# Kernel optimization log

Measured on AMD Instinct MI355X. Metric: run time of the kernel, lower is better.

Reference implementation:

```python
import jax, jax.numpy as jnp
import numpy as np


def gcn_conv(x, W, b, src, dst, n_nodes):
    """PyG GCNConv: linear transform, then symmetric-normalized sparse aggregation.
    src/dst already include self-loops. Messages flow src -> dst."""
    xw = x @ W  # [N, out]
    deg = jax.ops.segment_sum(jnp.ones_like(dst, dtype=xw.dtype), dst, num_segments=n_nodes)
    dinv = jnp.where(deg > 0, jax.lax.rsqrt(deg), 0.0)
    norm = dinv[src] * dinv[dst]  # [E]
    msg = xw[src] * norm[:, None]  # gather + scale
    out = jax.ops.segment_sum(msg, dst, num_segments=n_nodes)  # scatter-add
    return out + b


def setup_inputs() -> dict:
    key = jax.random.key(0)
    ks = jax.random.split(key, 5)
    N, E, C_in, C_out = 50000, 800000, 512, 128
    H = 2 * C_out
    x = jax.random.normal(ks[0], (N, C_in), dtype=jnp.float32)
    edge_index = jax.random.randint(ks[1], (2, E), 0, N, dtype=jnp.int64)
    def glorot(k, shape):
        lim = float(np.sqrt(6.0 / (shape[0] + shape[1])))
        return jax.random.uniform(k, shape, jnp.float32, -lim, lim)
    return {
        "x": x,
        "edge_index": edge_index,
        "W1": glorot(ks[2], (C_in, H)),
        "b1": jnp.zeros((H,), jnp.float32),
        "W_mu": glorot(ks[3], (H, C_out)),
        "b_mu": jnp.zeros((C_out,), jnp.float32),
        "W_ls": glorot(ks[4], (H, C_out)),
        "b_ls": jnp.zeros((C_out,), jnp.float32),
    }


def reference(x, edge_index, W1, b1, W_mu, b_mu, W_ls, b_ls):
    n_nodes = x.shape[0]
    # add self-loops (PyG GCNConv default add_self_loops=True)
    loops = jnp.arange(n_nodes, dtype=edge_index.dtype)
    src = jnp.concatenate([edge_index[0], loops])
    dst = jnp.concatenate([edge_index[1], loops])
    h = jax.nn.relu(gcn_conv(x, W1, b1, src, dst, n_nodes))
    mu = gcn_conv(h, W_mu, b_mu, src, dst, n_nodes)
    logstd = gcn_conv(h, W_ls, b_ls, src, dst, n_nodes)
    # stack so output is a single array [2, N, out_channels]
    return jnp.stack([mu, logstd])
```

## Files before the change

kernel.cpp:

```cpp
#include <hip/hip_runtime.h>

static inline int ceil_div(int a, int b) { return (a + b - 1) / b; }

typedef __attribute__((ext_vector_type(8))) __bf16 bf16x8;
typedef __attribute__((ext_vector_type(8))) unsigned short ushort8;
typedef __attribute__((ext_vector_type(4))) float f32x4;

#define ELLPAD 64

__device__ __forceinline__ unsigned short f2bf(float f) {
    union { float f; unsigned u; } v; v.f = f;
    unsigned r = v.u + 0x7fffu + ((v.u >> 16) & 1u);
    return (unsigned short)(r >> 16);
}
__device__ __forceinline__ float blo(unsigned u) {
    union { unsigned u; float f; } x; x.u = u << 16; return x.f;
}
__device__ __forceinline__ float bhi(unsigned u) {
    union { unsigned u; float f; } x; x.u = u & 0xffff0000u; return x.f;
}

#define SWZ(r) ((((r) & 3) ^ (((r) >> 2) & 3)))

typedef __attribute__((address_space(3))) unsigned lds_uint;
typedef __attribute__((address_space(1))) const unsigned glb_uint;
__device__ __forceinline__ void gload_lds16(const unsigned short* g, unsigned short* l) {
    __builtin_amdgcn_global_load_lds((glb_uint*)g, (lds_uint*)l, 16, 0, 0);
}

__global__ __launch_bounds__(256) void k_prep(const int* __restrict__ src, const int* __restrict__ dst,
                                              int E, int* __restrict__ cnt, int* __restrict__ ell, int N,
                                              const float* __restrict__ x, unsigned short* __restrict__ xb,
                                              long nx,
                                              const float* __restrict__ W1, const float* __restrict__ Wmu,
                                              const float* __restrict__ Wls, unsigned short* __restrict__ W1t,
                                              unsigned short* __restrict__ Wct, int K1, int H, int Cout,
                                              int nbE, int nbX, int ilv) {
    const int b = blockIdx.x;
    int phase, idx;
    if (b < nbE + nbX) {
        if (ilv) {
            if ((b % 5) == 0 && (b / 5) < nbE) { phase = 0; idx = b / 5; }
            else { phase = 1; idx = b - min(b / 5 + 1, nbE); }
        } else {
            if (b < nbE) { phase = 0; idx = b; }
            else { phase = 1; idx = b - nbE; }
        }
    } else { phase = 2; idx = b - nbE - nbX; }

    if (phase == 0) {
        const int e = idx * 256 + threadIdx.x;
        if (e < E) {
            const int d = dst[e];
            const int r = atomicAdd(&cnt[d], 1);
            if (r < ELLPAD) ell[(size_t)d * ELLPAD + r] = src[e];
        }
    } else if (phase == 1) {
        long i = (long)idx * 2048 + (long)threadIdx.x * 8;
        if (i < nx) {
            float4 a0 = *(const float4*)(x + i);
            float4 a1 = *(const float4*)(x + i + 4);
            ushort8 t;
            t[0] = f2bf(a0.x); t[1] = f2bf(a0.y); t[2] = f2bf(a0.z); t[3] = f2bf(a0.w);
            t[4] = f2bf(a1.x); t[5] = f2bf(a1.y); t[6] = f2bf(a1.z); t[7] = f2bf(a1.w);
            *(ushort8*)(xb + i) = t;
        }
    } else {
        int t = idx * 256 + threadIdx.x;
        int n1 = H * K1;
        int n2 = 2 * Cout * H;
        if (t < n1) {
            int c = t / K1, k = t - c * K1;
            W1t[t] = f2bf(W1[(size_t)k * H + c]);
        } else if (t < n1 + n2) {
            int u = t - n1;
            int c = u / H, k = u - c * H;
            float v = (c < Cout) ? Wmu[(size_t)k * Cout + c] : Wls[(size_t)k * Cout + (c - Cout)];
            Wct[u] = f2bf(v);
        }
    }
}

__device__ __forceinline__ void gemm_tile_core(const unsigned short* __restrict__ A,
                                               const unsigned short* __restrict__ B,
                                               unsigned short* __restrict__ As, unsigned short* __restrict__ Bs,
                                               int row0, int col0, int K,
                                               int wave, int lane, f32x4 (*acc)[4]) {
    const int quad = lane >> 4, l16 = lane & 15;
    const int rw = wave & 1, cw = wave >> 1;
    const int srow = wave * 32 + (lane >> 2);
    const int slot = lane & 3;
    for (int k0 = 0; k0 < K; k0 += 32) {
#pragma unroll
        for (int t = 0; t < 2; ++t) {
            const int lr = srow + t * 16;
            const int kc = (slot ^ SWZ(lr)) * 8;
            gload_lds16(A + (size_t)(row0 + lr) * K + k0 + kc, As + (wave * 32 + t * 16) * 32);
            gload_lds16(B + (size_t)(col0 + lr) * K + k0 + kc, Bs + (wave * 32 + t * 16) * 32);
        }
        __syncthreads();
        bf16x8 af[4], bf[4];
#pragma unroll
        for (int i = 0; i < 4; ++i) {
            const int lr = rw * 64 + i * 16 + l16;
            af[i] = *(const bf16x8*)&As[lr * 32 + ((quad ^ SWZ(lr))) * 8];
            const int lc = cw * 64 + i * 16 + l16;
            bf[i] = *(const bf16x8*)&Bs[lc * 32 + ((quad ^ SWZ(lc))) * 8];
        }
#pragma unroll
        for (int i = 0; i < 4; ++i)
#pragma unroll
            for (int j = 0; j < 4; ++j)
                acc[i][j] = __builtin_amdgcn_mfma_f32_16x16x32_bf16(af[i], bf[j], acc[i][j], 0, 0, 0);
        __syncthreads();
    }
}

__global__ __launch_bounds__(256) void k_gemm1(const unsigned short* __restrict__ xb,
                                               const unsigned short* __restrict__ W1t,
                                               unsigned short* __restrict__ y, int N, int K,
                                               const int* __restrict__ cnt, float* __restrict__ dinv) {
    __shared__ __align__(16) unsigned short As[128 * 32];
    __shared__ __align__(16) unsigned short Bs[128 * 32];
    const int tid = threadIdx.x, wave = tid >> 6, lane = tid & 63;
    const int quad = lane >> 4, l16 = lane & 15;
    const int row0 = blockIdx.x * 128, col0 = blockIdx.y * 128;
    if (blockIdx.y == 0 && tid < 128) {
        const int i = row0 + tid;
        if (i < N) dinv[i] = rsqrtf((float)(cnt[i] + 1));
    }
    const int rw = wave & 1, cw = wave >> 1;
    f32x4 acc[4][4] = {};
    gemm_tile_core(xb, W1t, As, Bs, row0, col0, K, wave, lane, acc);
#pragma unroll
    for (int i = 0; i < 4; ++i) {
        const int grb = row0 + rw * 64 + i * 16 + quad * 4;
#pragma unroll
        for (int r = 0; r < 4; ++r) {
            const int row = grb + r;
            if (row < N) {
#pragma unroll
                for (int j = 0; j < 4; ++j)
                    y[(size_t)row * 256 + col0 + cw * 64 + j * 16 + l16] = f2bf(acc[i][j][r]);
            }
        }
    }
}

__global__ __launch_bounds__(256) void k_gemm2(const unsigned short* __restrict__ g,
                                               const unsigned short* __restrict__ Wct,
                                               const float* __restrict__ bmu, const float* __restrict__ bls,
                                               float* __restrict__ out, int N, int Cout) {
    __shared__ __align__(16) unsigned short As[128 * 32];
    __shared__ __align__(16) unsigned short Bs[128 * 32];
    const int K = 256;
    const int tid = threadIdx.x, wave = tid >> 6, lane = tid & 63;
    const int quad = lane >> 4, l16 = lane & 15;
    const int row0 = blockIdx.x * 128, col0 = blockIdx.y * 128;
    const int rw = wave & 1, cw = wave >> 1;
    f32x4 acc[4][4] = {};
    gemm_tile_core(g, Wct, As, Bs, row0, col0, K, wave, lane, acc);
#pragma unroll
    for (int j = 0; j < 4; ++j) {
        const int c = col0 + cw * 64 + j * 16 + l16;
        const bool is_mu = (c < Cout);
        const int ocl = is_mu ? c : (c - Cout);
        const float bv = is_mu ? bmu[ocl] : bls[ocl];
        const size_t obase = is_mu ? 0 : (size_t)N * Cout;
#pragma unroll
        for (int i = 0; i < 4; ++i) {
            const int grb = row0 + rw * 64 + i * 16 + quad * 4;
#pragma unroll
            for (int r = 0; r < 4; ++r) {
                const int row = grb + r;
                if (row < N) out[obase + (size_t)row * Cout + ocl] = acc[i][j][r] + bv;
            }
        }
    }
}

__global__ __launch_bounds__(256) void k_agg(const unsigned short* __restrict__ Yin,
                                             const int* __restrict__ ell, const int* __restrict__ cnt,
                                             const float* __restrict__ dinv, const float* __restrict__ bias,
                                             unsigned short* __restrict__ Yout, int N, int relu_mode) {
    const int n = blockIdx.x * 4 + (threadIdx.x >> 6);
    if (n >= N) return;
    const int lane = threadIdx.x & 63;
    const int c = lane * 4;
    const int L = min(cnt[n], ELLPAD);
    const int* __restrict__ col = ell + (size_t)n * ELLPAD;
    const float dn = dinv[n];
    const uint2 vn = *(const uint2*)(Yin + (size_t)n * 256 + c);
    float ax0 = dn * blo(vn.x), ay0 = dn * bhi(vn.x), az0 = dn * blo(vn.y), aw0 = dn * bhi(vn.y);
    float ax1 = 0.f, ay1 = 0.f, az1 = 0.f, aw1 = 0.f;
    int j = 0;
    for (; j + 3 < L; j += 4) {
        const int s0 = col[j], s1 = col[j + 1], s2 = col[j + 2], s3 = col[j + 3];
        const float d0 = dinv[s0], d1 = dinv[s1], d2 = dinv[s2], d3 = dinv[s3];
        const uint2 v0 = *(const uint2*)(Yin + (size_t)s0 * 256 + c);
        const uint2 v1 = *(const uint2*)(Yin + (size_t)s1 * 256 + c);
        const uint2 v2 = *(const uint2*)(Yin + (size_t)s2 * 256 + c);
        const uint2 v3 = *(const uint2*)(Yin + (size_t)s3 * 256 + c);
        ax0 = fmaf(d0, blo(v0.x), fmaf(d1, blo(v1.x), ax0));
        ay0 = fmaf(d0, bhi(v0.x), fmaf(d1, bhi(v1.x), ay0));
        az0 = fmaf(d0, blo(v0.y), fmaf(d1, blo(v1.y), az0));
        aw0 = fmaf(d0, bhi(v0.y), fmaf(d1, bhi(v1.y), aw0));
        ax1 = fmaf(d2, blo(v2.x), fmaf(d3, blo(v3.x), ax1));
        ay1 = fmaf(d2, bhi(v2.x), fmaf(d3, bhi(v3.x), ay1));
        az1 = fmaf(d2, blo(v2.y), fmaf(d3, blo(v3.y), az1));
        aw1 = fmaf(d2, bhi(v2.y), fmaf(d3, bhi(v3.y), aw1));
    }
    for (; j < L; ++j) {
        const int s0 = col[j];
        const float d0 = dinv[s0];
        const uint2 v0 = *(const uint2*)(Yin + (size_t)s0 * 256 + c);
        ax0 = fmaf(d0, blo(v0.x), ax0);
        ay0 = fmaf(d0, bhi(v0.x), ay0);
        az0 = fmaf(d0, blo(v0.y), az0);
        aw0 = fmaf(d0, bhi(v0.y), aw0);
    }
    const float ax = ax0 + ax1, ay = ay0 + ay1, az = az0 + az1, aw = aw0 + aw1;
    float ox, oy, oz, ow;
    if (relu_mode) {
        const float4 b = *(const float4*)&bias[c];
        ox = fmaxf(fmaf(dn, ax, b.x), 0.f);
        oy = fmaxf(fmaf(dn, ay, b.y), 0.f);
        oz = fmaxf(fmaf(dn, az, b.z), 0.f);
        ow = fmaxf(fmaf(dn, aw, b.w), 0.f);
    } else {
        ox = dn * ax; oy = dn * ay; oz = dn * az; ow = dn * aw;
    }
    uint2 o;
    o.x = (unsigned)f2bf(ox) | ((unsigned)f2bf(oy) << 16);
    o.y = (unsigned)f2bf(oz) | ((unsigned)f2bf(ow) << 16);
    *(uint2*)(Yout + (size_t)n * 256 + c) = o;
}


extern "C" void kernel_launch(void* const* d_in, const int* in_sizes, int n_in,
                              void* d_out, int out_size, void* d_ws, size_t ws_size,
                              hipStream_t stream) {
    const float* x   = (const float*)d_in[0];
    const int*   ei  = (const int*)d_in[1];
    const float* W1  = (const float*)d_in[2];
    const float* b1  = (const float*)d_in[3];
    const float* Wmu = (const float*)d_in[4];
    const float* bmu = (const float*)d_in[5];
    const float* Wls = (const float*)d_in[6];
    const float* bls = (const float*)d_in[7];

    const int H    = in_sizes[3];
    const int Cin  = in_sizes[2] / H;
    const int Cout = in_sizes[5];
    const int N    = in_sizes[0] / Cin;
    const int E    = in_sizes[1] / 2;
    const int* srcv = ei;
    const int* dstv = ei + E;

    char* w = (char*)d_ws;
    size_t off = 0;
    auto alloc = [&](size_t bytes) -> void* {
        void* p = w + off;
        off = (off + bytes + 255) & ~(size_t)255;
        return p;
    };
    int*            cnt  = (int*)alloc((size_t)N * 4);
    float*          dinv = (float*)alloc((size_t)N * 4);
    int*            ell  = (int*)alloc((size_t)N * ELLPAD * 4);
    unsigned short* W1t  = (unsigned short*)alloc((size_t)H * Cin * 2);
    unsigned short* Wct  = (unsigned short*)alloc((size_t)2 * Cout * H * 2);
    unsigned short* xb   = (unsigned short*)alloc((size_t)N * Cin * 2);
    unsigned short* y    = (unsigned short*)alloc((size_t)N * H * 2);
    unsigned short* y2   = (unsigned short*)alloc((size_t)(N + 128) * H * 2);
    unsigned short* g    = y;
    (void)ws_size; (void)n_in; (void)out_size;

    hipMemsetAsync(cnt, 0, (size_t)N * 4, stream);

    const long nx = (long)N * Cin;
    const int nbE = ceil_div(E, 256);
    const int nbX = (int)((nx + 2047) / 2048);
    const int nbW = ceil_div(H * Cin + 2 * Cout * H, 256);
    const int ilv = (nbX == 4 * nbE) ? 1 : 0;
    k_prep<<<nbE + nbX + nbW, 256, 0, stream>>>(srcv, dstv, E, cnt, ell, N, x, xb, nx,
                                                W1, Wmu, Wls, W1t, Wct, Cin, H, Cout, nbE, nbX, ilv);

    dim3 g1(ceil_div(N, 128), 2);
    k_gemm1<<<g1, 256, 0, stream>>>(xb, W1t, y, N, Cin, cnt, dinv);

    k_agg<<<ceil_div(N, 4), 256, 0, stream>>>(y, ell, cnt, dinv, b1, y2, N, 1);
    k_agg<<<ceil_div(N, 4), 256, 0, stream>>>(y2, ell, cnt, dinv, nullptr, g, N, 0);

    dim3 g2(ceil_div(N, 128), 2);
    k_gemm2<<<g2, 256, 0, stream>>>(g, Wct, bmu, bls, (float*)d_out, N, Cout);
}
```

Baseline: 375.4 us.

## Build ELL adjacency via bucketed counting sort instead of global atomics

Replaces the per-edge global atomicAdd ELL construction with a multi-pass bucket partition: per-block LDS histograms of destination buckets, a scan over them, a partition pass that writes (src,dst) pairs grouped by bucket, then a per-bucket kernel that counts degrees and fills the ELL rows with LDS atomics. This targets contention from scattered global atomics and uncoalesced ELL writes, and removes the memset and the dinv computation inside the GEMM. In exchange it adds three kernel launches and an extra pass over the edges through a pair buffer. Row order inside ELL is still nondeterministic, and the ELL buffer is sized to a multiple of the bucket width.

```diff
diff --git a/kernel.cpp b/kernel.cpp
--- a/kernel.cpp
+++ b/kernel.cpp
@@ -7,6 +7,10 @@
 typedef __attribute__((ext_vector_type(4))) float f32x4;
 
 #define ELLPAD 64
+#define SH 7
+#define NPB 128
+#define NBLK 256
+#define MAXBUCK 512
 
 __device__ __forceinline__ unsigned short f2bf(float f) {
     union { float f; unsigned u; } v; v.f = f;
@@ -28,35 +32,26 @@
     __builtin_amdgcn_global_load_lds((glb_uint*)g, (lds_uint*)l, 16, 0, 0);
 }
 
-__global__ __launch_bounds__(256) void k_prep(const int* __restrict__ src, const int* __restrict__ dst,
-                                              int E, int* __restrict__ cnt, int* __restrict__ ell, int N,
+__global__ __launch_bounds__(256) void k_prep(const int* __restrict__ dst, int E, int NBUCK, int CE,
+                                              int* __restrict__ h,
                                               const float* __restrict__ x, unsigned short* __restrict__ xb,
                                               long nx,
                                               const float* __restrict__ W1, const float* __restrict__ Wmu,
                                               const float* __restrict__ Wls, unsigned short* __restrict__ W1t,
                                               unsigned short* __restrict__ Wct, int K1, int H, int Cout,
-                                              int nbE, int nbX, int ilv) {
+                                              int nbX) {
     const int b = blockIdx.x;
-    int phase, idx;
-    if (b < nbE + nbX) {
-        if (ilv) {
-            if ((b % 5) == 0 && (b / 5) < nbE) { phase = 0; idx = b / 5; }
-            else { phase = 1; idx = b - min(b / 5 + 1, nbE); }
-        } else {
-            if (b < nbE) { phase = 0; idx = b; }
-            else { phase = 1; idx = b - nbE; }
-        }
-    } else { phase = 2; idx = b - nbE - nbX; }
-
-    if (phase == 0) {
-        const int e = idx * 256 + threadIdx.x;
-        if (e < E) {
-            const int d = dst[e];
-            const int r = atomicAdd(&cnt[d], 1);
-            if (r < ELLPAD) ell[(size_t)d * ELLPAD + r] = src[e];
-        }
-    } else if (phase == 1) {
-        long i = (long)idx * 2048 + (long)threadIdx.x * 8;
+    const int tid = threadIdx.x;
+    if (b < NBLK) {
+        __shared__ int shist[MAXBUCK];
+        for (int i = tid; i < NBUCK; i += 256) shist[i] = 0;
+        __syncthreads();
+        const int e0 = b * CE, e1 = min(e0 + CE, E);
+        for (int e = e0 + tid; e < e1; e += 256) atomicAdd(&shist[dst[e] >> SH], 1);
+        __syncthreads();
+        for (int i = tid; i < NBUCK; i += 256) h[(size_t)b * NBUCK + i] = shist[i];
+    } else if (b < NBLK + nbX) {
+        long i = (long)(b - NBLK) * 2048 + (long)tid * 8;
         if (i < nx) {
             float4 a0 = *(const float4*)(x + i);
             float4 a1 = *(const float4*)(x + i + 4);
@@ -66,7 +61,7 @@
             *(ushort8*)(xb + i) = t;
         }
     } else {
-        int t = idx * 256 + threadIdx.x;
+        int t = (b - NBLK - nbX) * 256 + tid;
         int n1 = H * K1;
         int n2 = 2 * Cout * H;
         if (t < n1) {
@@ -81,6 +76,93 @@
     }
 }
 
+__global__ __launch_bounds__(256) void k_scan1(int* __restrict__ h, int* __restrict__ tot, int NBUCK) {
+    __shared__ int ws[5];
+    const int bkt = blockIdx.x, tid = threadIdx.x;
+    const int lane = tid & 63, wave = tid >> 6;
+    const int v = h[(size_t)tid * NBUCK + bkt];
+    int x = v;
+    for (int off = 1; off < 64; off <<= 1) {
+        int t = __shfl_up(x, off);
+        if (lane >= off) x += t;
+    }
+    if (lane == 63) ws[wave] = x;
+    __syncthreads();
+    if (tid == 0) {
+        int r = 0;
+        for (int k = 0; k < 4; ++k) { int t = ws[k]; ws[k] = r; r += t; }
+        ws[4] = r;
+        tot[bkt] = r;
+    }
+    __syncthreads();
+    h[(size_t)tid * NBUCK + bkt] = ws[wave] + x - v;
+}
+
+__global__ __launch_bounds__(512) void k_part(const int* __restrict__ src, const int* __restrict__ dst,
+                                              int E, int NBUCK, int CE,
+                                              const int* __restrict__ h, const int* __restrict__ tot,
+                                              int2* __restrict__ pair) {
+    __shared__ int sT[MAXBUCK + 1];
+    __shared__ int cur[MAXBUCK];
+    const int blk = blockIdx.x, tid = threadIdx.x;
+    if (tid <= NBUCK) sT[tid] = (tid == 0) ? 0 : tot[tid - 1];
+    __syncthreads();
+    for (int off = 1; off <= NBUCK; off <<= 1) {
+        int v = 0;
+        if (tid <= NBUCK && tid >= off) v = sT[tid - off];
+        __syncthreads();
+        if (tid <= NBUCK && tid >= off) sT[tid] += v;
+        __syncthreads();
+    }
+    if (tid < NBUCK) cur[tid] = sT[tid] + h[(size_t)blk * NBUCK + tid];
+    __syncthreads();
+    const int e0 = blk * CE, e1 = min(e0 + CE, E);
+    for (int e = e0 + tid; e < e1; e += 512) {
+        const int d = dst[e];
+        const int p = atomicAdd(&cur[d >> SH], 1);
+        pair[p] = make_int2(src[e], d);
+    }
+}
+
+__global__ __launch_bounds__(256) void k_ell(const int2* __restrict__ pair, const int* __restrict__ tot,
+                                             int NBUCK, int N,
+                                             int* __restrict__ ell, int* __restrict__ cnt,
+                                             float* __restrict__ dinv) {
+    __shared__ int lhist[NPB];
+    __shared__ int ws[4];
+    __shared__ int sbase;
+    const int bkt = blockIdx.x, tid = threadIdx.x;
+    const int lane = tid & 63, wave = tid >> 6;
+    int part = 0;
+    for (int i = tid; i < bkt; i += 256) part += tot[i];
+    for (int off = 32; off > 0; off >>= 1) part += __shfl_down(part, off);
+    if (lane == 0) ws[wave] = part;
+    if (tid < NPB) lhist[tid] = 0;
+    __syncthreads();
+    if (tid == 0) sbase = ws[0] + ws[1] + ws[2] + ws[3];
+    __syncthreads();
+    const int base = sbase;
+    const int len = tot[bkt];
+    for (int i = base + tid; i < base + len; i += 256) atomicAdd(&lhist[pair[i].y & (NPB - 1)], 1);
+    __syncthreads();
+    if (tid < NPB) {
+        const int node = (bkt << SH) + tid;
+        if (node < N) {
+            const int c = lhist[tid];
+            cnt[node] = c;
+            dinv[node] = rsqrtf((float)(c + 1));
+        }
+        lhist[tid] = 0;
+    }
+    __syncthreads();
+    for (int i = base + tid; i < base + len; i += 256) {
+        const int2 e = pair[i];
+        const int ln = e.y & (NPB - 1);
+        const int p = atomicAdd(&lhist[ln], 1);
+        if (p < ELLPAD) ell[(size_t)e.y * ELLPAD + p] = e.x;
+    }
+}
+
 __device__ __forceinline__ void gemm_tile_core(const unsigned short* __restrict__ A,
                                                const unsigned short* __restrict__ B,
                                                unsigned short* __restrict__ As, unsigned short* __restrict__ Bs,
@@ -118,17 +200,12 @@
 
 __global__ __launch_bounds__(256) void k_gemm1(const unsigned short* __restrict__ xb,
                                                const unsigned short* __restrict__ W1t,
-                                               unsigned short* __restrict__ y, int N, int K,
-                                               const int* __restrict__ cnt, float* __restrict__ dinv) {
+                                               unsigned short* __restrict__ y, int N, int K) {
     __shared__ __align__(16) unsigned short As[128 * 32];
     __shared__ __align__(16) unsigned short Bs[128 * 32];
     const int tid = threadIdx.x, wave = tid >> 6, lane = tid & 63;
     const int quad = lane >> 4, l16 = lane & 15;
     const int row0 = blockIdx.x * 128, col0 = blockIdx.y * 128;
-    if (blockIdx.y == 0 && tid < 128) {
-        const int i = row0 + tid;
-        if (i < N) dinv[i] = rsqrtf((float)(cnt[i] + 1));
-    }
     const int rw = wave & 1, cw = wave >> 1;
     f32x4 acc[4][4] = {};
     gemm_tile_core(xb, W1t, As, Bs, row0, col0, K, wave, lane, acc);
@@ -264,9 +341,14 @@
         off = (off + bytes + 255) & ~(size_t)255;
         return p;
     };
+    const int NBUCK = (N + NPB - 1) >> SH;
+    const int CE = ceil_div(E, NBLK);
+    int*            hh   = (int*)alloc((size_t)NBLK * NBUCK * 4);
+    int*            tot  = (int*)alloc((size_t)NBUCK * 4);
+    int2*           pair = (int2*)alloc((size_t)E * 8);
     int*            cnt  = (int*)alloc((size_t)N * 4);
     float*          dinv = (float*)alloc((size_t)N * 4);
-    int*            ell  = (int*)alloc((size_t)N * ELLPAD * 4);
+    int*            ell  = (int*)alloc((size_t)(NBUCK * NPB) * ELLPAD * 4);
     unsigned short* W1t  = (unsigned short*)alloc((size_t)H * Cin * 2);
     unsigned short* Wct  = (unsigned short*)alloc((size_t)2 * Cout * H * 2);
     unsigned short* xb   = (unsigned short*)alloc((size_t)N * Cin * 2);
@@ -275,18 +357,18 @@
     unsigned short* g    = y;
     (void)ws_size; (void)n_in; (void)out_size;
 
-    hipMemsetAsync(cnt, 0, (size_t)N * 4, stream);
-
     const long nx = (long)N * Cin;
-    const int nbE = ceil_div(E, 256);
     const int nbX = (int)((nx + 2047) / 2048);
     const int nbW = ceil_div(H * Cin + 2 * Cout * H, 256);
-    const int ilv = (nbX == 4 * nbE) ? 1 : 0;
-    k_prep<<<nbE + nbX + nbW, 256, 0, stream>>>(srcv, dstv, E, cnt, ell, N, x, xb, nx,
-                                                W1, Wmu, Wls, W1t, Wct, Cin, H, Cout, nbE, nbX, ilv);
+
+    k_prep<<<NBLK + nbX + nbW, 256, 0, stream>>>(dstv, E, NBUCK, CE, hh, x, xb, nx,
+                                                 W1, Wmu, Wls, W1t, Wct, Cin, H, Cout, nbX);
+    k_scan1<<<NBUCK, 256, 0, stream>>>(hh, tot, NBUCK);
+    k_part<<<NBLK, 512, 0, stream>>>(srcv, dstv, E, NBUCK, CE, hh, tot, pair);
+    k_ell<<<NBUCK, 256, 0, stream>>>(pair, tot, NBUCK, N, ell, cnt, dinv);
 
     dim3 g1(ceil_div(N, 128), 2);
-    k_gemm1<<<g1, 256, 0, stream>>>(xb, W1t, y, N, Cin, cnt, dinv);
+    k_gemm1<<<g1, 256, 0, stream>>>(xb, W1t, y, N, Cin);
 
     k_agg<<<ceil_div(N, 4), 256, 0, stream>>>(y, ell, cnt, dinv, b1, y2, N, 1);
     k_agg<<<ceil_div(N, 4), 256, 0, stream>>>(y2, ell, cnt, dinv, nullptr, g, N, 0);
```

Result: no change. 380.5 us (+1.4%).
